# Kernel optimization log

Measured on AMD Instinct MI355X. Metric: run time of the kernel, lower is better.

The kernel has to match this reference:

```python
import jax, jax.numpy as jnp
import numpy as np

NEG_INF = -1e30


def _rope_interleaved(x, freqs):
    # x: [B,S,H,D], freqs broadcastable [1,S,1,D]; interleaved even/odd rotation
    x0 = x[..., 0::2]
    x1 = x[..., 1::2]
    f0 = freqs[..., 0::2]
    f1 = freqs[..., 1::2]
    o0 = f0 * x0 - f1 * x1
    o1 = f1 * x0 + f0 * x1
    # interleave back: out[...,0::2]=o0, out[...,1::2]=o1
    out = jnp.stack([o0, o1], axis=-1)  # [B,S,H,D/2,2]
    return out.reshape(x.shape).astype(x.dtype)


def setup_inputs() -> dict:
    key = jax.random.key(0)
    kq, kk, kv, kf = jax.random.split(key, 4)
    B, S, H, D = 2, 2048, 16, 128
    q = jax.random.normal(kq, (B, S, H, D), dtype=jnp.float32)
    k = jax.random.normal(kk, (B, S, H, D), dtype=jnp.float32)
    v = jax.random.normal(kv, (B, S, H, D), dtype=jnp.float32)
    freqs = jax.random.normal(kf, (1, S, 1, D), dtype=jnp.float32)
    return {"q": q, "k": k, "v": v, "freqs": freqs}


def reference(q, k, v, freqs):
    # RoPE (Wan-style indexed interleaved write) on q and k
    rq = _rope_interleaved(q, freqs)  # [B,S,H,D]
    rk = _rope_interleaved(k, freqs)
    B, S, H, D = q.shape
    scale = 1.0 / jnp.sqrt(jnp.asarray(D, dtype=q.dtype))
    # transpose(1,2) -> [B,H,S,D]; fused into einsum subscripts
    scores = jnp.einsum("bqhd,bkhd->bhqk", rq, rk) * scale  # [B,H,S,S]
    causal = jnp.tril(jnp.ones((S, S), dtype=bool))
    scores = jnp.where(causal[None, None, :, :], scores, NEG_INF)
    probs = jax.nn.softmax(scores, axis=-1)
    out = jnp.einsum("bhqk,bkhd->bhqd", probs, v)  # [B,H,S,D]
    return out
```

## Files before the change

kernel.cpp:

```cpp
#include <hip/hip_runtime.h>
#include <hip/hip_bf16.h>

#define B_  2
#define S_  2048
#define H_  16
#define D_  128
#define BQ  128
#define BK  64
#define SH  (H_ * D_)
#define NT  (S_ / 64)
#define NTQ (S_ / BQ)
#define TILE_US 8192

typedef __attribute__((ext_vector_type(8))) short bf16x8;
typedef __attribute__((ext_vector_type(4))) float f32x4;

__device__ __forceinline__ ushort f2bf(float x) {
  union { float f; unsigned u; } c; c.f = x;
  unsigned u = c.u;
  return (ushort)((u + 0x7FFFu + ((u >> 16) & 1u)) >> 16);
}

__device__ __forceinline__ void gload_lds16(const ushort* g, ushort* l) {
  __builtin_amdgcn_global_load_lds((const __attribute__((address_space(1))) void*)g,
                                   (__attribute__((address_space(3))) void*)l,
                                   16, 0, 0);
}

__global__ __launch_bounds__(256)
void pack_all(const float* __restrict__ qg, const float* __restrict__ kg,
              const float* __restrict__ vg, const float* __restrict__ fg,
              ushort* __restrict__ qr, ushort* __restrict__ kr,
              ushort* __restrict__ vt) {
  __shared__ float sv[64][133];
  const int t = blockIdx.x, h = blockIdx.y, b = blockIdx.z;
  const int tid = threadIdx.x;
  const float QS = 0.08838834764831845f * 1.4426950408889634f;
  const size_t tbase = ((size_t)(b * H_ + h) * NT + t) * TILE_US;

  #pragma unroll
  for (int c = 0; c < 4; c++) {
    const int idx = tid + 256 * c;
    const int row = idx >> 4;
    const int cu  = idx & 15;
    const int col = cu * 8;
    const int s   = t * 64 + row;
    const size_t goff = ((size_t)(b * S_ + s)) * SH + (size_t)h * D_ + col;

    const float4 f0 = *(const float4*)(fg + (size_t)s * D_ + col);
    const float4 f1 = *(const float4*)(fg + (size_t)s * D_ + col + 4);
    const float4 qx0 = *(const float4*)(qg + goff);
    const float4 qx1 = *(const float4*)(qg + goff + 4);
    const float4 kx0 = *(const float4*)(kg + goff);
    const float4 kx1 = *(const float4*)(kg + goff + 4);
    const float4 vx0 = *(const float4*)(vg + goff);
    const float4 vx1 = *(const float4*)(vg + goff + 4);

    *(float4*)&sv[row][col]     = vx0;
    *(float4*)&sv[row][col + 4] = vx1;

    union { ushort s[8]; uint4 v; } pq, pk;
    pq.s[0] = f2bf((f0.x*qx0.x - f0.y*qx0.y) * QS);
    pq.s[1] = f2bf((f0.y*qx0.x + f0.x*qx0.y) * QS);
    pq.s[2] = f2bf((f0.z*qx0.z - f0.w*qx0.w) * QS);
    pq.s[3] = f2bf((f0.w*qx0.z + f0.z*qx0.w) * QS);
    pq.s[4] = f2bf((f1.x*qx1.x - f1.y*qx1.y) * QS);
    pq.s[5] = f2bf((f1.y*qx1.x + f1.x*qx1.y) * QS);
    pq.s[6] = f2bf((f1.z*qx1.z - f1.w*qx1.w) * QS);
    pq.s[7] = f2bf((f1.w*qx1.z + f1.z*qx1.w) * QS);
    pk.s[0] = f2bf(f0.x*kx0.x - f0.y*kx0.y);
    pk.s[1] = f2bf(f0.y*kx0.x + f0.x*kx0.y);
    pk.s[2] = f2bf(f0.z*kx0.z - f0.w*kx0.w);
    pk.s[3] = f2bf(f0.w*kx0.z + f0.z*kx0.w);
    pk.s[4] = f2bf(f1.x*kx1.x - f1.y*kx1.y);
    pk.s[5] = f2bf(f1.y*kx1.x + f1.x*kx1.y);
    pk.s[6] = f2bf(f1.z*kx1.z - f1.w*kx1.w);
    pk.s[7] = f2bf(f1.w*kx1.z + f1.z*kx1.w);

    const int pos = ((cu >> 2) * 4 + (row >> 4)) * 64 + ((row & 15) | ((cu & 3) << 4));
    *(uint4*)(qr + tbase + (size_t)pos * 8) = pq.v;
    *(uint4*)(kr + tbase + (size_t)pos * 8) = pk.v;
  }
  __syncthreads();

  #pragma unroll
  for (int c = 0; c < 4; c++) {
    const int u2  = tid + 256 * c;
    const int g2  = u2 >> 6;
    const int ln  = u2 & 63;
    const int dim = (g2 & 7) * 16 + (ln & 15);
    const int k0  = (g2 >> 3) * 32 + (ln >> 4) * 8;
    union { ushort s[8]; uint4 v; } p;
    #pragma unroll
    for (int j = 0; j < 8; j++) p.s[j] = f2bf(sv[k0 + j][dim]);
    *(uint4*)(vt + tbase + (size_t)u2 * 8) = p.v;
  }
}

__global__ __launch_bounds__(256, 2)
void fattn4(const ushort* __restrict__ qr, const ushort* __restrict__ kr,
            const ushort* __restrict__ vt, float* __restrict__ og) {
  __shared__ __align__(16) ushort sK[2][TILE_US];
  __shared__ __align__(16) ushort sV[2][TILE_US];
  __shared__ __align__(16) ushort sP[4][2048];

  const int qt   = NTQ - 1 - (int)blockIdx.x;
  const int h    = blockIdx.y;
  const int b    = blockIdx.z;
  const int tid  = threadIdx.x;
  const int wv   = tid >> 6;
  const int lane = tid & 63;
  const int l15  = lane & 15;
  const int quad = lane >> 4;

  const size_t bh = (size_t)(b * H_ + h);
  const ushort* ktb = kr + bh * NT * TILE_US;
  const ushort* vtb = vt + bh * NT * TILE_US;

  bf16x8 afq[2][4];
  {
    const ushort* qtb64 = qr + (bh * NT + 2 * qt + (wv >> 1)) * TILE_US;
    const int rbb = (wv & 1) * 2;
    #pragma unroll
    for (int rh = 0; rh < 2; rh++)
      #pragma unroll
      for (int ks = 0; ks < 4; ks++)
        afq[rh][ks] = *(const bf16x8*)(qtb64 + (size_t)((ks * 4 + rbb + rh) * 64 + lane) * 8);
  }

  float rs[2][4];
  f32x4 o_acc[2][8];
  #pragma unroll
  for (int rh = 0; rh < 2; rh++) {
    #pragma unroll
    for (int r = 0; r < 4; r++) rs[rh][r] = 0.0f;
    #pragma unroll
    for (int dt = 0; dt < 8; dt++) o_acc[rh][dt] = (f32x4)0.0f;
  }

  #pragma unroll
  for (int c = 0; c < 4; c++) {
    const int g = wv * 4 + c;
    gload_lds16(ktb + g * 512 + lane * 8, &sK[0][g * 512 + lane * 8]);
    gload_lds16(vtb + g * 512 + lane * 8, &sV[0][g * 512 + lane * 8]);
  }

  const int nkt = 2 * qt + 2;
  int buf = 0;
  for (int kt = 0; kt < nkt; kt++) {
    __syncthreads();

    if (kt + 1 < nkt) {
      const ushort* ksrc = ktb + (size_t)(kt + 1) * TILE_US;
      const ushort* vsrc = vtb + (size_t)(kt + 1) * TILE_US;
      #pragma unroll
      for (int c = 0; c < 4; c++) {
        const int g = wv * 4 + c;
        gload_lds16(ksrc + g * 512 + lane * 8, &sK[buf ^ 1][g * 512 + lane * 8]);
        gload_lds16(vsrc + g * 512 + lane * 8, &sV[buf ^ 1][g * 512 + lane * 8]);
      }
    }

    f32x4 sc[2][4];
    #pragma unroll
    for (int rh = 0; rh < 2; rh++)
      #pragma unroll
      for (int nt = 0; nt < 4; nt++) sc[rh][nt] = (f32x4)0.0f;
    #pragma unroll
    for (int nt = 0; nt < 4; nt++) {
      #pragma unroll
      for (int ks = 0; ks < 4; ks++) {
        const bf16x8 bk_ = *(const bf16x8*)&sK[buf][(size_t)((ks * 4 + nt) * 64 + lane) * 8];
        sc[0][nt] = __builtin_amdgcn_mfma_f32_16x16x32_bf16(afq[0][ks], bk_, sc[0][nt], 0, 0, 0);
        sc[1][nt] = __builtin_amdgcn_mfma_f32_16x16x32_bf16(afq[1][ks], bk_, sc[1][nt], 0, 0, 0);
      }
    }

    if (kt >= 2 * qt) {
      #pragma unroll
      for (int rh = 0; rh < 2; rh++) {
        #pragma unroll
        for (int nt = 0; nt < 4; nt++) {
          const int col = kt * 64 + nt * 16 + l15;
          #pragma unroll
          for (int r = 0; r < 4; r++) {
            const int row = qt * 128 + wv * 32 + rh * 16 + quad * 4 + r;
            if (col > row) sc[rh][nt][r] = -1e30f;
          }
        }
      }
    }

    #pragma unroll
    for (int rh = 0; rh < 2; rh++) {
      #pragma unroll
      for (int nt = 0; nt < 4; nt++) {
        const int base = rh * 1024 + (nt >> 1) * 512
                       + (((nt & 1) << 1) | (l15 >> 3)) * 128 + (l15 & 7);
        #pragma unroll
        for (int r = 0; r < 4; r++) {
          const float p = __builtin_amdgcn_exp2f(sc[rh][nt][r]);
          rs[rh][r] += p;
          sP[wv][base + (quad * 4 + r) * 8] = f2bf(p);
        }
      }
    }

    bf16x8 ap[2][2];
    #pragma unroll
    for (int rh = 0; rh < 2; rh++)
      #pragma unroll
      for (int ks = 0; ks < 2; ks++)
        ap[rh][ks] = *(const bf16x8*)&sP[wv][(size_t)(rh * 1024 + (ks * 64 + lane) * 8)];
    #pragma unroll
    for (int dt = 0; dt < 8; dt++) {
      #pragma unroll
      for (int ks = 0; ks < 2; ks++) {
        const bf16x8 bv = *(const bf16x8*)&sV[buf][(size_t)((ks * 8 + dt) * 64 + lane) * 8];
        o_acc[0][dt] = __builtin_amdgcn_mfma_f32_16x16x32_bf16(ap[0][ks], bv, o_acc[0][dt], 0, 0, 0);
        o_acc[1][dt] = __builtin_amdgcn_mfma_f32_16x16x32_bf16(ap[1][ks], bv, o_acc[1][dt], 0, 0, 0);
      }
    }

    buf ^= 1;
  }

  float* ob = og + (bh * S_ + (size_t)qt * BQ) * D_;
  #pragma unroll
  for (int rh = 0; rh < 2; rh++) {
    #pragma unroll
    for (int r = 0; r < 4; r++) {
      float t = rs[rh][r];
      t += __shfl_xor(t, 1);
      t += __shfl_xor(t, 2);
      t += __shfl_xor(t, 4);
      t += __shfl_xor(t, 8);
      const float inv = 1.0f / t;
      const int row = wv * 32 + rh * 16 + quad * 4 + r;
      #pragma unroll
      for (int dt = 0; dt < 8; dt++)
        ob[(size_t)row * D_ + dt * 16 + l15] = o_acc[rh][dt][r] * inv;
    }
  }
}

extern "C" void kernel_launch(void* const* d_in, const int* in_sizes, int n_in,
                              void* d_out, int out_size, void* d_ws, size_t ws_size,
                              hipStream_t stream) {
  const float* q = (const float*)d_in[0];
  const float* k = (const float*)d_in[1];
  const float* v = (const float*)d_in[2];
  const float* f = (const float*)d_in[3];
  float* o = (float*)d_out;

  const size_t NELT = (size_t)B_ * S_ * H_ * D_;
  ushort* qr = (ushort*)d_ws;
  ushort* kr = qr + NELT;
  ushort* vt = kr + NELT;

  dim3 block(256);
  pack_all<<<dim3(NT, H_, B_), block, 0, stream>>>(q, k, v, f, qr, kr, vt);
  fattn4<<<dim3(NTQ, H_, B_), block, 0, stream>>>(qr, kr, vt, o);
}
```

Baseline: 214.2 us.

## Fuse Q RoPE into attention kernel and read K/V directly from global

Moves the Q rotary embedding and bf16 packing out of the pack kernel into the attention kernel's prologue, so the packed Q workspace is neither written nor read back. The attention kernel drops its double-buffered LDS staging of K/V tiles and the per-tile barriers, loading MFMA operands straight from global memory. With the smaller LDS footprint it can target 3 blocks per CU, and it uses a flattened 1D grid ordered heaviest-query-tile first across all heads. The trade-off is that K/V loads now depend on L1/L2 hits and no longer overlap with compute through explicit prefetch.

Result: slower. 348.9 us (+62.9%).

```diff
diff --git a/kernel.cpp b/kernel.cpp
--- a/kernel.cpp
+++ b/kernel.cpp
@@ -6,7 +6,6 @@
 #define H_  16
 #define D_  128
 #define BQ  128
-#define BK  64
 #define SH  (H_ * D_)
 #define NT  (S_ / 64)
 #define NTQ (S_ / BQ)
@@ -21,21 +20,13 @@
   return (ushort)((u + 0x7FFFu + ((u >> 16) & 1u)) >> 16);
 }
 
-__device__ __forceinline__ void gload_lds16(const ushort* g, ushort* l) {
-  __builtin_amdgcn_global_load_lds((const __attribute__((address_space(1))) void*)g,
-                                   (__attribute__((address_space(3))) void*)l,
-                                   16, 0, 0);
-}
-
 __global__ __launch_bounds__(256)
-void pack_all(const float* __restrict__ qg, const float* __restrict__ kg,
-              const float* __restrict__ vg, const float* __restrict__ fg,
-              ushort* __restrict__ qr, ushort* __restrict__ kr,
-              ushort* __restrict__ vt) {
+void pack_kv(const float* __restrict__ kg, const float* __restrict__ vg,
+             const float* __restrict__ fg,
+             ushort* __restrict__ kr, ushort* __restrict__ vt) {
   __shared__ float sv[64][133];
   const int t = blockIdx.x, h = blockIdx.y, b = blockIdx.z;
   const int tid = threadIdx.x;
-  const float QS = 0.08838834764831845f * 1.4426950408889634f;
   const size_t tbase = ((size_t)(b * H_ + h) * NT + t) * TILE_US;
 
   #pragma unroll
@@ -49,8 +40,6 @@
 
     const float4 f0 = *(const float4*)(fg + (size_t)s * D_ + col);
     const float4 f1 = *(const float4*)(fg + (size_t)s * D_ + col + 4);
-    const float4 qx0 = *(const float4*)(qg + goff);
-    const float4 qx1 = *(const float4*)(qg + goff + 4);
     const float4 kx0 = *(const float4*)(kg + goff);
     const float4 kx1 = *(const float4*)(kg + goff + 4);
     const float4 vx0 = *(const float4*)(vg + goff);
@@ -59,15 +48,7 @@
     *(float4*)&sv[row][col]     = vx0;
     *(float4*)&sv[row][col + 4] = vx1;
 
-    union { ushort s[8]; uint4 v; } pq, pk;
-    pq.s[0] = f2bf((f0.x*qx0.x - f0.y*qx0.y) * QS);
-    pq.s[1] = f2bf((f0.y*qx0.x + f0.x*qx0.y) * QS);
-    pq.s[2] = f2bf((f0.z*qx0.z - f0.w*qx0.w) * QS);
-    pq.s[3] = f2bf((f0.w*qx0.z + f0.z*qx0.w) * QS);
-    pq.s[4] = f2bf((f1.x*qx1.x - f1.y*qx1.y) * QS);
-    pq.s[5] = f2bf((f1.y*qx1.x + f1.x*qx1.y) * QS);
-    pq.s[6] = f2bf((f1.z*qx1.z - f1.w*qx1.w) * QS);
-    pq.s[7] = f2bf((f1.w*qx1.z + f1.z*qx1.w) * QS);
+    union { ushort s[8]; uint4 v; } pk;
     pk.s[0] = f2bf(f0.x*kx0.x - f0.y*kx0.y);
     pk.s[1] = f2bf(f0.y*kx0.x + f0.x*kx0.y);
     pk.s[2] = f2bf(f0.z*kx0.z - f0.w*kx0.w);
@@ -78,7 +59,6 @@
     pk.s[7] = f2bf(f1.w*kx1.z + f1.z*kx1.w);
 
     const int pos = ((cu >> 2) * 4 + (row >> 4)) * 64 + ((row & 15) | ((cu & 3) << 4));
-    *(uint4*)(qr + tbase + (size_t)pos * 8) = pq.v;
     *(uint4*)(kr + tbase + (size_t)pos * 8) = pk.v;
   }
   __syncthreads();
@@ -97,35 +77,54 @@
   }
 }
 
-__global__ __launch_bounds__(256, 2)
-void fattn4(const ushort* __restrict__ qr, const ushort* __restrict__ kr,
-            const ushort* __restrict__ vt, float* __restrict__ og) {
-  __shared__ __align__(16) ushort sK[2][TILE_US];
-  __shared__ __align__(16) ushort sV[2][TILE_US];
+__global__ __launch_bounds__(256, 3)
+void fattn5(const float* __restrict__ qg, const float* __restrict__ fg,
+            const ushort* __restrict__ kr, const ushort* __restrict__ vt,
+            float* __restrict__ og) {
   __shared__ __align__(16) ushort sP[4][2048];
 
-  const int qt   = NTQ - 1 - (int)blockIdx.x;
-  const int h    = blockIdx.y;
-  const int b    = blockIdx.z;
+  const int idx  = (int)blockIdx.x;
+  const int qt   = NTQ - 1 - (idx >> 5);
+  const int bh   = idx & 31;
+  const int b    = bh >> 4;
+  const int h    = bh & 15;
   const int tid  = threadIdx.x;
   const int wv   = tid >> 6;
   const int lane = tid & 63;
   const int l15  = lane & 15;
   const int quad = lane >> 4;
 
-  const size_t bh = (size_t)(b * H_ + h);
-  const ushort* ktb = kr + bh * NT * TILE_US;
-  const ushort* vtb = vt + bh * NT * TILE_US;
+  const size_t bhs = (size_t)bh;
+  const ushort* ktb = kr + bhs * NT * TILE_US;
+  const ushort* vtb = vt + bhs * NT * TILE_US;
+  const float QS = 0.08838834764831845f * 1.4426950408889634f;
 
   bf16x8 afq[2][4];
   {
-    const ushort* qtb64 = qr + (bh * NT + 2 * qt + (wv >> 1)) * TILE_US;
-    const int rbb = (wv & 1) * 2;
-    #pragma unroll
-    for (int rh = 0; rh < 2; rh++)
-      #pragma unroll
-      for (int ks = 0; ks < 4; ks++)
-        afq[rh][ks] = *(const bf16x8*)(qtb64 + (size_t)((ks * 4 + rbb + rh) * 64 + lane) * 8);
+    const float* qb = qg + ((size_t)b * S_ + (size_t)qt * BQ) * SH + (size_t)h * D_;
+    #pragma unroll
+    for (int rh = 0; rh < 2; rh++) {
+      const int row = wv * 32 + rh * 16 + l15;
+      const int s   = qt * BQ + row;
+      #pragma unroll
+      for (int ks = 0; ks < 4; ks++) {
+        const int d0 = ks * 32 + quad * 8;
+        const float4 x0 = *(const float4*)(qb + (size_t)row * SH + d0);
+        const float4 x1 = *(const float4*)(qb + (size_t)row * SH + d0 + 4);
+        const float4 f0 = *(const float4*)(fg + (size_t)s * D_ + d0);
+        const float4 f1 = *(const float4*)(fg + (size_t)s * D_ + d0 + 4);
+        union { ushort u[8]; bf16x8 v; } pq;
+        pq.u[0] = f2bf((f0.x*x0.x - f0.y*x0.y) * QS);
+        pq.u[1] = f2bf((f0.y*x0.x + f0.x*x0.y) * QS);
+        pq.u[2] = f2bf((f0.z*x0.z - f0.w*x0.w) * QS);
+        pq.u[3] = f2bf((f0.w*x0.z + f0.z*x0.w) * QS);
+        pq.u[4] = f2bf((f1.x*x1.x - f1.y*x1.y) * QS);
+        pq.u[5] = f2bf((f1.y*x1.x + f1.x*x1.y) * QS);
+        pq.u[6] = f2bf((f1.z*x1.z - f1.w*x1.w) * QS);
+        pq.u[7] = f2bf((f1.w*x1.z + f1.z*x1.w) * QS);
+        afq[rh][ks] = pq.v;
+      }
+    }
   }
 
   float rs[2][4];
@@ -138,28 +137,10 @@
     for (int dt = 0; dt < 8; dt++) o_acc[rh][dt] = (f32x4)0.0f;
   }
 
-  #pragma unroll
-  for (int c = 0; c < 4; c++) {
-    const int g = wv * 4 + c;
-    gload_lds16(ktb + g * 512 + lane * 8, &sK[0][g * 512 + lane * 8]);
-    gload_lds16(vtb + g * 512 + lane * 8, &sV[0][g * 512 + lane * 8]);
-  }
-
   const int nkt = 2 * qt + 2;
-  int buf = 0;
   for (int kt = 0; kt < nkt; kt++) {
-    __syncthreads();
-
-    if (kt + 1 < nkt) {
-      const ushort* ksrc = ktb + (size_t)(kt + 1) * TILE_US;
-      const ushort* vsrc = vtb + (size_t)(kt + 1) * TILE_US;
-      #pragma unroll
-      for (int c = 0; c < 4; c++) {
-        const int g = wv * 4 + c;
-        gload_lds16(ksrc + g * 512 + lane * 8, &sK[buf ^ 1][g * 512 + lane * 8]);
-        gload_lds16(vsrc + g * 512 + lane * 8, &sV[buf ^ 1][g * 512 + lane * 8]);
-      }
-    }
+    const ushort* kp = ktb + (size_t)kt * TILE_US;
+    const ushort* vp = vtb + (size_t)kt * TILE_US;
 
     f32x4 sc[2][4];
     #pragma unroll
@@ -170,9 +151,9 @@
     for (int nt = 0; nt < 4; nt++) {
       #pragma unroll
       for (int ks = 0; ks < 4; ks++) {
-        const bf16x8 bk_ = *(const bf16x8*)&sK[buf][(size_t)((ks * 4 + nt) * 64 + lane) * 8];
-        sc[0][nt] = __builtin_amdgcn_mfma_f32_16x16x32_bf16(afq[0][ks], bk_, sc[0][nt], 0, 0, 0);
-        sc[1][nt] = __builtin_amdgcn_mfma_f32_16x16x32_bf16(afq[1][ks], bk_, sc[1][nt], 0, 0, 0);
+        const bf16x8 bk = *(const bf16x8*)(kp + (size_t)((ks * 4 + nt) * 64 + lane) * 8);
+        sc[0][nt] = __builtin_amdgcn_mfma_f32_16x16x32_bf16(afq[0][ks], bk, sc[0][nt], 0, 0, 0);
+        sc[1][nt] = __builtin_amdgcn_mfma_f32_16x16x32_bf16(afq[1][ks], bk, sc[1][nt], 0, 0, 0);
       }
     }
 
@@ -184,7 +165,7 @@
           const int col = kt * 64 + nt * 16 + l15;
           #pragma unroll
           for (int r = 0; r < 4; r++) {
-            const int row = qt * 128 + wv * 32 + rh * 16 + quad * 4 + r;
+            const int row = qt * BQ + wv * 32 + rh * 16 + quad * 4 + r;
             if (col > row) sc[rh][nt][r] = -1e30f;
           }
         }
@@ -216,16 +197,14 @@
     for (int dt = 0; dt < 8; dt++) {
       #pragma unroll
       for (int ks = 0; ks < 2; ks++) {
-        const bf16x8 bv = *(const bf16x8*)&sV[buf][(size_t)((ks * 8 + dt) * 64 + lane) * 8];
+        const bf16x8 bv = *(const bf16x8*)(vp + (size_t)((ks * 8 + dt) * 64 + lane) * 8);
         o_acc[0][dt] = __builtin_amdgcn_mfma_f32_16x16x32_bf16(ap[0][ks], bv, o_acc[0][dt], 0, 0, 0);
         o_acc[1][dt] = __builtin_amdgcn_mfma_f32_16x16x32_bf16(ap[1][ks], bv, o_acc[1][dt], 0, 0, 0);
       }
     }
-
-    buf ^= 1;
-  }
-
-  float* ob = og + (bh * S_ + (size_t)qt * BQ) * D_;
+  }
+
+  float* ob = og + (bhs * S_ + (size_t)qt * BQ) * D_;
   #pragma unroll
   for (int rh = 0; rh < 2; rh++) {
     #pragma unroll
@@ -254,11 +233,10 @@
   float* o = (float*)d_out;
 
   const size_t NELT = (size_t)B_ * S_ * H_ * D_;
-  ushort* qr = (ushort*)d_ws;
-  ushort* kr = qr + NELT;
+  ushort* kr = (ushort*)d_ws;
   ushort* vt = kr + NELT;
 
   dim3 block(256);
-  pack_all<<<dim3(NT, H_, B_), block, 0, stream>>>(q, k, v, f, qr, kr, vt);
-  fattn4<<<dim3(NTQ, H_, B_), block, 0, stream>>>(qr, kr, vt, o);
-}
+  pack_kv<<<dim3(NT, H_, B_), block, 0, stream>>>(k, v, f, kr, vt);
+  fattn5<<<dim3(NTQ * 32, 1, 1), block, 0, stream>>>(q, f, kr, vt, o);
+}
```
